# Performance work log

Measured on AMD Instinct MI355X. Metric: run time of the kernel, lower is better.

The kernel has to match this reference:

```python
import jax, jax.numpy as jnp
import numpy as np

SR = 48000
MAX_DUR = 5.0
N_AUDIO = 480000  # 10 s @ 48 kHz
K_IR = int(SR * MAX_DUR)  # 240000 taps


def setup_inputs() -> dict:
    key = jax.random.key(0)
    k1, k2 = jax.random.split(key)
    audio = jax.random.normal(k1, (N_AUDIO,), dtype=jnp.float32)
    impulse_response = jax.random.normal(k2, (K_IR,), dtype=jnp.float32)
    return {"audio": audio, "impulse_response": impulse_response}


def reference(audio, impulse_response):
    # torch: pad audio with (K-1) zeros, then conv1d (= cross-correlation, no flip)
    K = impulse_response.shape[0]
    a_pad = jnp.concatenate([audio, jnp.zeros((K - 1,), dtype=audio.dtype)])
    # out[t] = sum_k a_pad[t+k] * ir[k], valid correlation -> length N
    out = jnp.correlate(a_pad, impulse_response, mode="valid")
    # trailing peak normalization
    return out / jnp.max(jnp.abs(out))
```

## Files before the change

### kernel.cpp

```cpp
#include <hip/hip_runtime.h>
#include <hip/hip_bf16.h>

typedef unsigned int u32;


constexpr int N_AUDIO = 480000;
constexpr int K_IR    = 240000;
constexpr int M_FFT   = 1048576;

constexpr size_t OFF_C0   = 0;
constexpr size_t OFF_C1   = (size_t)M_FFT * 8;
constexpr size_t OFF_SLOT = OFF_C1 + (size_t)M_FFT * 8;

__device__ __forceinline__ float2 cmul(float2 a, float2 b) {
    return make_float2(a.x * b.x - a.y * b.y, a.x * b.y + a.y * b.x);
}
__device__ __forceinline__ float2 twid(float frac) {
    float s, c;
    __sincosf(-6.28318530717958647692f * frac, &s, &c);
    return make_float2(c, s);
}

__device__ __forceinline__ void build_tw(float2* tw, int t) {
    for (int i = t + 1; i < 1024; i += 256) {
        int L = 1 << (31 - __builtin_clz(i));
        tw[i] = twid((float)(i - L) / (float)(2 * L));
    }
}

__device__ __forceinline__ void fft1024x2(float2 (*src)[1024], float2 (*scr)[1024],
                                          const float2* tw, int t) {
    float2 (*A)[1024] = src;
    float2 (*B)[1024] = scr;
    #pragma unroll
    for (int s = 0; s < 10; ++s) {
        const int L = 1 << s;
        #pragma unroll
        for (int h = 0; h < 2; ++h) {
            const int tid = t + 256 * h;
            const int k   = tid & (L - 1);
            const float2 w = tw[L + k];
            const int o0  = 2 * tid - k;
            #pragma unroll
            for (int j = 0; j < 2; ++j) {
                float2 x0 = A[j][tid];
                float2 x1 = A[j][tid + 512];
                float2 t1 = cmul(w, x1);
                B[j][o0]     = make_float2(x0.x + t1.x, x0.y + t1.y);
                B[j][o0 + L] = make_float2(x0.x - t1.x, x0.y - t1.y);
            }
        }
        __syncthreads();
        float2 (*tmp)[1024] = A; A = B; B = tmp;
    }
}

__global__ __launch_bounds__(256) void fft1_pass1(const float* __restrict__ a,
                                                  const float* __restrict__ b,
                                                  float2* __restrict__ outb,
                                                  u32* __restrict__ slot) {
    __shared__ float2 rows[2][1024];
    __shared__ float2 scr [2][1024];
    __shared__ float2 tw[1024];
    const int t  = threadIdx.x;
    const int r0 = blockIdx.x * 2;
    if (blockIdx.x == 0 && t == 0) *slot = 0u;
    build_tw(tw, t);
    #pragma unroll
    for (int q = 0; q < 4; ++q) {
        int c = t + 256 * q;
        int base = c * 1024 + r0;
        float2 av = make_float2(0.f, 0.f), bv = make_float2(0.f, 0.f);
        if (c < 468 || (c == 468 && r0 < 768)) av = *(const float2*)(a + base);
        if (c < 234 || (c == 234 && r0 < 384)) bv = *(const float2*)(b + base);
        rows[0][c] = make_float2(av.x, bv.x);
        rows[1][c] = make_float2(av.y, bv.y);
    }
    __syncthreads();
    fft1024x2(rows, scr, tw, t);
    #pragma unroll
    for (int q = 0; q < 4; ++q) {
        int i2 = t + 256 * q;
        int j  = i2 >> 9;
        int k1 = (i2 & 511) * 2;
        float fr = (float)(r0 + j) * (1.0f / 1048576.0f);
        float2 e0 = cmul(twid(fr * (float)k1),       rows[j][k1]);
        float2 e1 = cmul(twid(fr * (float)(k1 + 1)), rows[j][k1 + 1]);
        ((float4*)outb)[r0 * 512 + i2] = make_float4(e0.x, e0.y, e1.x, e1.y);
    }
}

__global__ __launch_bounds__(256) void fft1_pass2_pw(const float2* __restrict__ in,
                                                     float2* __restrict__ spec) {
    __shared__ float2 cols[2][1024];
    __shared__ float2 scr [2][1024];
    __shared__ float2 tw[1024];
    const int t = threadIdx.x;
    const int bidx = blockIdx.x;
    const int cA = (bidx == 0) ? 0   : bidx;
    const int cB = (bidx == 0) ? 512 : 1024 - bidx;
    build_tw(tw, t);
    #pragma unroll
    for (int q = 0; q < 4; ++q) {
        int r = t + 256 * q;
        cols[0][r] = in[r * 1024 + cA];
        cols[1][r] = in[r * 1024 + cB];
    }
    __syncthreads();
    fft1024x2(cols, scr, tw, t);
    const float invM = 1.0f / 1048576.0f;
    #pragma unroll
    for (int q = 0; q < 4; ++q) {
        int k2 = t + 256 * q;
        #pragma unroll
        for (int j = 0; j < 2; ++j) {
            float2 z1 = cols[j][k2];
            float2 z2;
            if (bidx == 0) z2 = (j == 0) ? cols[0][(1024 - k2) & 1023]
                                         : cols[1][1023 - k2];
            else           z2 = cols[j ^ 1][1023 - k2];
            float2 Af = make_float2(0.5f * (z1.x + z2.x), 0.5f * (z1.y - z2.y));
            float2 cB2 = make_float2(0.5f * (z1.y + z2.y), 0.5f * (z1.x - z2.x));
            float2 S  = cmul(Af, cB2);
            int cc = (j == 0) ? cA : cB;
            spec[cc * 1024 + k2] = make_float2(S.x * invM, -S.y * invM);
        }
    }
}

__global__ __launch_bounds__(256) void fft2_pass1(const float2* __restrict__ in,
                                                  float2* __restrict__ outb) {
    __shared__ float2 rows[2][1024];
    __shared__ float2 scr [2][1024];
    __shared__ float2 tw[1024];
    const int t  = threadIdx.x;
    const int r0 = blockIdx.x * 2;
    build_tw(tw, t);
    const float4* inv4 = (const float4*)(in + (size_t)r0 * 1024);
    #pragma unroll
    for (int q = 0; q < 4; ++q) {
        int i2 = t + 256 * q;
        float4 v = inv4[i2];
        int j = i2 >> 9, c = (i2 & 511) * 2;
        rows[j][c]     = make_float2(v.x, v.y);
        rows[j][c + 1] = make_float2(v.z, v.w);
    }
    __syncthreads();
    fft1024x2(rows, scr, tw, t);
    #pragma unroll
    for (int q = 0; q < 4; ++q) {
        int i2 = t + 256 * q;
        int j  = i2 >> 9;
        int k1 = (i2 & 511) * 2;
        float fr = (float)(r0 + j) * (1.0f / 1048576.0f);
        float2 e0 = cmul(twid(fr * (float)k1),       rows[j][k1]);
        float2 e1 = cmul(twid(fr * (float)(k1 + 1)), rows[j][k1 + 1]);
        ((float4*)outb)[r0 * 512 + i2] = make_float4(e0.x, e0.y, e1.x, e1.y);
    }
}

__global__ __launch_bounds__(256) void fft2_pass2(const float2* __restrict__ in,
                                                  float* __restrict__ raw,
                                                  u32* __restrict__ slot) {
    __shared__ float2 cols[2][1024];
    __shared__ float2 scr [2][1024];
    __shared__ float2 tw[1024];
    __shared__ float  wmax[4];
    const int t  = threadIdx.x;
    const int c0 = blockIdx.x * 2;
    build_tw(tw, t);
    #pragma unroll
    for (int q = 0; q < 4; ++q) {
        int r = t + 256 * q;
        float4 v = *(const float4*)(in + (size_t)r * 1024 + c0);
        cols[0][r] = make_float2(v.x, v.y);
        cols[1][r] = make_float2(v.z, v.w);
    }
    __syncthreads();
    fft1024x2(cols, scr, tw, t);
    float m = 0.0f;
    #pragma unroll
    for (int q = 0; q < 8; ++q) {
        int idx = t + 256 * q;
        int jj = idx & 1, k2 = idx >> 1;
        int ot = c0 + jj + (k2 << 10);
        if (ot < N_AUDIO) {
            float v = cols[jj][k2].x;
            raw[ot] = v;
            m = fmaxf(m, fabsf(v));
        }
    }
    for (int off = 32; off > 0; off >>= 1) m = fmaxf(m, __shfl_down(m, off, 64));
    if ((t & 63) == 0) wmax[t >> 6] = m;
    __syncthreads();
    if (t == 0) {
        float bm = fmaxf(fmaxf(wmax[0], wmax[1]), fmaxf(wmax[2], wmax[3]));
        atomicMax(slot, __float_as_uint(bm));
    }
}

__global__ __launch_bounds__(256) void scale_k(const float* __restrict__ raw,
                                               const u32* __restrict__ slot,
                                               float* __restrict__ out) {
    int i = blockIdx.x * 256 + threadIdx.x;
    if (i < N_AUDIO) out[i] = raw[i] / __uint_as_float(*slot);
}

extern "C" void kernel_launch(void* const* d_in, const int* in_sizes, int n_in,
                              void* d_out, int out_size, void* d_ws, size_t ws_size,
                              hipStream_t stream) {
    const float* audio = (const float*)d_in[0];
    const float* ir    = (const float*)d_in[1];
    float* out = (float*)d_out;

    char* ws = (char*)d_ws;
    float2* cb0 = (float2*)(ws + OFF_C0);
    float2* cb1 = (float2*)(ws + OFF_C1);
    u32*    slot = (u32*)(ws + OFF_SLOT);

    fft1_pass1<<<512, 256, 0, stream>>>(audio, ir, cb1, slot);
    fft1_pass2_pw<<<512, 256, 0, stream>>>(cb1, cb0);
    fft2_pass1<<<512, 256, 0, stream>>>(cb0, cb1);
    fft2_pass2<<<512, 256, 0, stream>>>(cb1, (float*)cb0, slot);
    scale_k<<<1875, 256, 0, stream>>>((const float*)cb0, slot, out);
}
```

Baseline: 112.5 us.

## Switch 1024-point FFTs to radix-4 with padded LDS and one row per block

Replaces the ten radix-2 Stockham stages with five radix-4 stages, which halves the shared-memory round trips and barriers per 1024-point transform. LDS indices are padded (i + i/16) to reduce bank conflicts. Three of the four FFT passes now handle one row or column per block over 1024 blocks instead of two per block over 512, which gives more blocks and a smaller LDS footprint. The cost is uncoalesced scalar loads in the column passes (fft2_p2 loads one float2 per row stride instead of a float4 pair) and more blocks each rebuilding the twiddle table.

```diff
diff --git a/kernel.cpp b/kernel.cpp
--- a/kernel.cpp
+++ b/kernel.cpp
@@ -1,5 +1,4 @@
 #include <hip/hip_runtime.h>
-#include <hip/hip_bf16.h>
 
 typedef unsigned int u32;
 
@@ -11,6 +10,9 @@
 constexpr size_t OFF_C0   = 0;
 constexpr size_t OFF_C1   = (size_t)M_FFT * 8;
 constexpr size_t OFF_SLOT = OFF_C1 + (size_t)M_FFT * 8;
+
+#define SW(i) ((i) + ((i) >> 4))
+constexpr int LSZ = 1088;
 
 __device__ __forceinline__ float2 cmul(float2 a, float2 b) {
     return make_float2(a.x * b.x - a.y * b.y, a.x * b.y + a.y * b.x);
@@ -20,81 +22,79 @@
     __sincosf(-6.28318530717958647692f * frac, &s, &c);
     return make_float2(c, s);
 }
-
 __device__ __forceinline__ void build_tw(float2* tw, int t) {
+    #pragma unroll
     for (int i = t + 1; i < 1024; i += 256) {
         int L = 1 << (31 - __builtin_clz(i));
         tw[i] = twid((float)(i - L) / (float)(2 * L));
     }
 }
 
-__device__ __forceinline__ void fft1024x2(float2 (*src)[1024], float2 (*scr)[1024],
-                                          const float2* tw, int t) {
-    float2 (*A)[1024] = src;
-    float2 (*B)[1024] = scr;
-    #pragma unroll
-    for (int s = 0; s < 10; ++s) {
-        const int L = 1 << s;
+template<int NB>
+__device__ __forceinline__ void fft1024_r4(float2 (*A0)[LSZ], float2 (*B0)[LSZ],
+                                           const float2* tw, int t) {
+    float2 (*A)[LSZ] = A0;
+    float2 (*B)[LSZ] = B0;
+    #pragma unroll
+    for (int s = 0; s < 5; ++s) {
+        const int L  = 1 << (2 * s);
+        const int k  = t & (L - 1);
+        const int p0 = 4 * t - 3 * k;
+        const float2 w  = tw[L + k];
+        const float2 w2 = tw[2 * L + k];
         #pragma unroll
-        for (int h = 0; h < 2; ++h) {
-            const int tid = t + 256 * h;
-            const int k   = tid & (L - 1);
-            const float2 w = tw[L + k];
-            const int o0  = 2 * tid - k;
-            #pragma unroll
-            for (int j = 0; j < 2; ++j) {
-                float2 x0 = A[j][tid];
-                float2 x1 = A[j][tid + 512];
-                float2 t1 = cmul(w, x1);
-                B[j][o0]     = make_float2(x0.x + t1.x, x0.y + t1.y);
-                B[j][o0 + L] = make_float2(x0.x - t1.x, x0.y - t1.y);
-            }
+        for (int j = 0; j < NB; ++j) {
+            float2 x0 = A[j][SW(t)];
+            float2 x2 = A[j][SW(t + 256)];
+            float2 x1 = A[j][SW(t + 512)];
+            float2 x3 = A[j][SW(t + 768)];
+            float2 wx1 = cmul(w, x1), wx3 = cmul(w, x3);
+            float2 u0 = make_float2(x0.x + wx1.x, x0.y + wx1.y);
+            float2 u1 = make_float2(x0.x - wx1.x, x0.y - wx1.y);
+            float2 u2 = make_float2(x2.x + wx3.x, x2.y + wx3.y);
+            float2 u3 = make_float2(x2.x - wx3.x, x2.y - wx3.y);
+            float2 a2 = cmul(w2, u2);
+            float2 a3 = cmul(w2, u3);
+            B[j][SW(p0)]         = make_float2(u0.x + a2.x, u0.y + a2.y);
+            B[j][SW(p0 + L)]     = make_float2(u1.x + a3.y, u1.y - a3.x);
+            B[j][SW(p0 + 2*L)]   = make_float2(u0.x - a2.x, u0.y - a2.y);
+            B[j][SW(p0 + 3*L)]   = make_float2(u1.x - a3.y, u1.y + a3.x);
         }
         __syncthreads();
-        float2 (*tmp)[1024] = A; A = B; B = tmp;
-    }
-}
-
-__global__ __launch_bounds__(256) void fft1_pass1(const float* __restrict__ a,
-                                                  const float* __restrict__ b,
-                                                  float2* __restrict__ outb,
-                                                  u32* __restrict__ slot) {
-    __shared__ float2 rows[2][1024];
-    __shared__ float2 scr [2][1024];
-    __shared__ float2 tw[1024];
-    const int t  = threadIdx.x;
-    const int r0 = blockIdx.x * 2;
-    if (blockIdx.x == 0 && t == 0) *slot = 0u;
+        float2 (*tmp)[LSZ] = A; A = B; B = tmp;
+    }
+}
+
+__global__ __launch_bounds__(256) void fft1_p1(const float* __restrict__ a,
+                                               const float* __restrict__ b,
+                                               float2* __restrict__ outb,
+                                               u32* __restrict__ slot) {
+    __shared__ float2 rows[1][LSZ], scr[1][LSZ], tw[1024];
+    const int t = threadIdx.x;
+    const int r = blockIdx.x;
+    if (r == 0 && t == 0) *slot = 0u;
     build_tw(tw, t);
     #pragma unroll
     for (int q = 0; q < 4; ++q) {
         int c = t + 256 * q;
-        int base = c * 1024 + r0;
-        float2 av = make_float2(0.f, 0.f), bv = make_float2(0.f, 0.f);
-        if (c < 468 || (c == 468 && r0 < 768)) av = *(const float2*)(a + base);
-        if (c < 234 || (c == 234 && r0 < 384)) bv = *(const float2*)(b + base);
-        rows[0][c] = make_float2(av.x, bv.x);
-        rows[1][c] = make_float2(av.y, bv.y);
-    }
-    __syncthreads();
-    fft1024x2(rows, scr, tw, t);
-    #pragma unroll
-    for (int q = 0; q < 4; ++q) {
-        int i2 = t + 256 * q;
-        int j  = i2 >> 9;
-        int k1 = (i2 & 511) * 2;
-        float fr = (float)(r0 + j) * (1.0f / 1048576.0f);
-        float2 e0 = cmul(twid(fr * (float)k1),       rows[j][k1]);
-        float2 e1 = cmul(twid(fr * (float)(k1 + 1)), rows[j][k1 + 1]);
-        ((float4*)outb)[r0 * 512 + i2] = make_float4(e0.x, e0.y, e1.x, e1.y);
-    }
-}
-
-__global__ __launch_bounds__(256) void fft1_pass2_pw(const float2* __restrict__ in,
-                                                     float2* __restrict__ spec) {
-    __shared__ float2 cols[2][1024];
-    __shared__ float2 scr [2][1024];
-    __shared__ float2 tw[1024];
+        int idx = c * 1024 + r;
+        float av = (idx < N_AUDIO) ? a[idx] : 0.0f;
+        float bv = (idx < K_IR)    ? b[idx] : 0.0f;
+        rows[0][SW(c)] = make_float2(av, bv);
+    }
+    __syncthreads();
+    fft1024_r4<1>(rows, scr, tw, t);
+    const float fr = (float)r * (1.0f / 1048576.0f);
+    #pragma unroll
+    for (int q = 0; q < 4; ++q) {
+        int k1 = t + 256 * q;
+        outb[r * 1024 + k1] = cmul(twid(fr * (float)k1), scr[0][SW(k1)]);
+    }
+}
+
+__global__ __launch_bounds__(256) void fft1_p2_pw(const float2* __restrict__ in,
+                                                  float2* __restrict__ spec) {
+    __shared__ float2 cols[2][LSZ], scr[2][LSZ], tw[1024];
     const int t = threadIdx.x;
     const int bidx = blockIdx.x;
     const int cA = (bidx == 0) ? 0   : bidx;
@@ -103,89 +103,74 @@
     #pragma unroll
     for (int q = 0; q < 4; ++q) {
         int r = t + 256 * q;
-        cols[0][r] = in[r * 1024 + cA];
-        cols[1][r] = in[r * 1024 + cB];
-    }
-    __syncthreads();
-    fft1024x2(cols, scr, tw, t);
+        cols[0][SW(r)] = in[r * 1024 + cA];
+        cols[1][SW(r)] = in[r * 1024 + cB];
+    }
+    __syncthreads();
+    fft1024_r4<2>(cols, scr, tw, t);
     const float invM = 1.0f / 1048576.0f;
     #pragma unroll
     for (int q = 0; q < 4; ++q) {
         int k2 = t + 256 * q;
         #pragma unroll
         for (int j = 0; j < 2; ++j) {
-            float2 z1 = cols[j][k2];
+            float2 z1 = scr[j][SW(k2)];
             float2 z2;
-            if (bidx == 0) z2 = (j == 0) ? cols[0][(1024 - k2) & 1023]
-                                         : cols[1][1023 - k2];
-            else           z2 = cols[j ^ 1][1023 - k2];
-            float2 Af = make_float2(0.5f * (z1.x + z2.x), 0.5f * (z1.y - z2.y));
-            float2 cB2 = make_float2(0.5f * (z1.y + z2.y), 0.5f * (z1.x - z2.x));
-            float2 S  = cmul(Af, cB2);
+            if (bidx == 0) z2 = (j == 0) ? scr[0][SW((1024 - k2) & 1023)]
+                                         : scr[1][SW(1023 - k2)];
+            else           z2 = scr[j ^ 1][SW(1023 - k2)];
+            float2 Af  = make_float2(0.5f * (z1.x + z2.x), 0.5f * (z1.y - z2.y));
+            float2 cBf = make_float2(0.5f * (z1.y + z2.y), 0.5f * (z1.x - z2.x));
+            float2 S   = cmul(Af, cBf);
             int cc = (j == 0) ? cA : cB;
             spec[cc * 1024 + k2] = make_float2(S.x * invM, -S.y * invM);
         }
     }
 }
 
-__global__ __launch_bounds__(256) void fft2_pass1(const float2* __restrict__ in,
-                                                  float2* __restrict__ outb) {
-    __shared__ float2 rows[2][1024];
-    __shared__ float2 scr [2][1024];
-    __shared__ float2 tw[1024];
-    const int t  = threadIdx.x;
-    const int r0 = blockIdx.x * 2;
-    build_tw(tw, t);
-    const float4* inv4 = (const float4*)(in + (size_t)r0 * 1024);
-    #pragma unroll
-    for (int q = 0; q < 4; ++q) {
-        int i2 = t + 256 * q;
-        float4 v = inv4[i2];
-        int j = i2 >> 9, c = (i2 & 511) * 2;
-        rows[j][c]     = make_float2(v.x, v.y);
-        rows[j][c + 1] = make_float2(v.z, v.w);
-    }
-    __syncthreads();
-    fft1024x2(rows, scr, tw, t);
-    #pragma unroll
-    for (int q = 0; q < 4; ++q) {
-        int i2 = t + 256 * q;
-        int j  = i2 >> 9;
-        int k1 = (i2 & 511) * 2;
-        float fr = (float)(r0 + j) * (1.0f / 1048576.0f);
-        float2 e0 = cmul(twid(fr * (float)k1),       rows[j][k1]);
-        float2 e1 = cmul(twid(fr * (float)(k1 + 1)), rows[j][k1 + 1]);
-        ((float4*)outb)[r0 * 512 + i2] = make_float4(e0.x, e0.y, e1.x, e1.y);
-    }
-}
-
-__global__ __launch_bounds__(256) void fft2_pass2(const float2* __restrict__ in,
-                                                  float* __restrict__ raw,
-                                                  u32* __restrict__ slot) {
-    __shared__ float2 cols[2][1024];
-    __shared__ float2 scr [2][1024];
-    __shared__ float2 tw[1024];
-    __shared__ float  wmax[4];
-    const int t  = threadIdx.x;
-    const int c0 = blockIdx.x * 2;
+__global__ __launch_bounds__(256) void fft2_p1(const float2* __restrict__ in,
+                                               float2* __restrict__ outb) {
+    __shared__ float2 rows[1][LSZ], scr[1][LSZ], tw[1024];
+    const int t = threadIdx.x;
+    const int r = blockIdx.x;
+    build_tw(tw, t);
+    #pragma unroll
+    for (int q = 0; q < 4; ++q) {
+        int c = t + 256 * q;
+        rows[0][SW(c)] = in[r * 1024 + c];
+    }
+    __syncthreads();
+    fft1024_r4<1>(rows, scr, tw, t);
+    const float fr = (float)r * (1.0f / 1048576.0f);
+    #pragma unroll
+    for (int q = 0; q < 4; ++q) {
+        int k1 = t + 256 * q;
+        outb[r * 1024 + k1] = cmul(twid(fr * (float)k1), scr[0][SW(k1)]);
+    }
+}
+
+__global__ __launch_bounds__(256) void fft2_p2(const float2* __restrict__ in,
+                                               float* __restrict__ raw,
+                                               u32* __restrict__ slot) {
+    __shared__ float2 cols[1][LSZ], scr[1][LSZ], tw[1024];
+    __shared__ float wmax[4];
+    const int t = threadIdx.x;
+    const int c = blockIdx.x;
     build_tw(tw, t);
     #pragma unroll
     for (int q = 0; q < 4; ++q) {
         int r = t + 256 * q;
-        float4 v = *(const float4*)(in + (size_t)r * 1024 + c0);
-        cols[0][r] = make_float2(v.x, v.y);
-        cols[1][r] = make_float2(v.z, v.w);
-    }
-    __syncthreads();
-    fft1024x2(cols, scr, tw, t);
+        cols[0][SW(r)] = in[r * 1024 + c];
+    }
+    __syncthreads();
+    fft1024_r4<1>(cols, scr, tw, t);
     float m = 0.0f;
     #pragma unroll
-    for (int q = 0; q < 8; ++q) {
-        int idx = t + 256 * q;
-        int jj = idx & 1, k2 = idx >> 1;
-        int ot = c0 + jj + (k2 << 10);
+    for (int q = 0; q < 4; ++q) {
+        int k2 = t + 256 * q;
+        int ot = c + (k2 << 10);
         if (ot < N_AUDIO) {
-            float v = cols[jj][k2].x;
+            float v = scr[0][SW(k2)].x;
             raw[ot] = v;
             m = fmaxf(m, fabsf(v));
         }
@@ -218,9 +203,9 @@
     float2* cb1 = (float2*)(ws + OFF_C1);
     u32*    slot = (u32*)(ws + OFF_SLOT);
 
-    fft1_pass1<<<512, 256, 0, stream>>>(audio, ir, cb1, slot);
-    fft1_pass2_pw<<<512, 256, 0, stream>>>(cb1, cb0);
-    fft2_pass1<<<512, 256, 0, stream>>>(cb0, cb1);
-    fft2_pass2<<<512, 256, 0, stream>>>(cb1, (float*)cb0, slot);
+    fft1_p1<<<1024, 256, 0, stream>>>(audio, ir, cb1, slot);
+    fft1_p2_pw<<<512, 256, 0, stream>>>(cb1, cb0);
+    fft2_p1<<<1024, 256, 0, stream>>>(cb0, cb1);
+    fft2_p2<<<1024, 256, 0, stream>>>(cb1, (float*)cb0, slot);
     scale_k<<<1875, 256, 0, stream>>>((const float*)cb0, slot, out);
 }
```

New measurement: 115.0 us. 1.02x slower.
